# Kernel optimization log

Measured on AMD Instinct MI355X. Metric: run time of the kernel, lower is better.

## Reference

```python
import jax, jax.numpy as jnp
import numpy as np

N = 150000      # active voxels
C = 64          # head input channels
KK = 9          # 3x3 kernel offsets
H = W = 700     # BEV feature map
BN_EPS = 1e-5
HEADS = [("heatmap", 3), ("center", 2), ("center_z", 1), ("dim", 3), ("rot", 2)]


def _build_neighbor_table(seed=0):
    """Submanifold 3x3 neighbor indices for N active voxels on an HxW grid.
    Entry -1 means the neighbor site is inactive (contributes zero)."""
    rng = np.random.default_rng(seed)
    flat = rng.choice(H * W, size=N, replace=False)
    ys, xs = flat // W, flat % W
    lut = np.full(H * W, -1, np.int64)
    lut[flat] = np.arange(N)
    nbr = np.full((N, KK), -1, np.int64)
    k = 0
    for dy in (-1, 0, 1):
        for dx in (-1, 0, 1):
            ny, nx = ys + dy, xs + dx
            valid = (ny >= 0) & (ny < H) & (nx >= 0) & (nx < W)
            nf = np.where(valid, ny * W + nx, 0)
            nbr[:, k] = np.where(valid, lut[nf], -1)
            k += 1
    return nbr


def setup_inputs() -> dict:
    key = jax.random.key(0)
    ks = jax.random.split(key, 2 + 2 * len(HEADS))
    inp = {
        "features": jax.random.normal(ks[0], (N, C), jnp.float32),
        "nbr_idx": jnp.asarray(_build_neighbor_table(), jnp.int32),
        # one 3x3 subm conv per head, stacked: [n_heads, 9, C_in, C_out]
        "W3": jax.random.normal(ks[1], (len(HEADS), KK, C, C), jnp.float32) * 0.05,
        "gamma": jnp.ones((len(HEADS), C), jnp.float32),
        "beta": jnp.zeros((len(HEADS), C), jnp.float32),
    }
    for i, (name, oc) in enumerate(HEADS):
        inp[f"W1_{name}"] = jax.random.normal(ks[2 + i], (C, oc), jnp.float32) * 0.001
        if name == "heatmap":
            inp[f"b1_{name}"] = jnp.full((oc,), -float(np.log((1 - 0.01) / 0.01)), jnp.float32)
        else:
            inp[f"b1_{name}"] = jnp.zeros((oc,), jnp.float32)
    return inp


def _forward(features, nbr_idx, W3, gamma, beta, W1s, b1s):
    valid = nbr_idx >= 0                                  # [N, 9]
    idx = jnp.where(valid, nbr_idx, 0)
    # gather active-neighbor features; missing neighbors -> zero (subm conv)
    gathered = features[idx] * valid[..., None].astype(features.dtype)  # [N, 9, C]
    # all heads share the same input sparse tensor -> batched gather-GEMM
    h = jnp.einsum('nkc,hkco->hno', gathered, W3)         # [n_heads, N, C]
    # BatchNorm1d (training-mode batch stats, biased var) + ReLU
    mean = h.mean(axis=1, keepdims=True)
    var = ((h - mean) ** 2).mean(axis=1, keepdims=True)
    hn = (h - mean) * jax.lax.rsqrt(var + BN_EPS)
    hn = jax.nn.relu(hn * gamma[:, None, :] + beta[:, None, :])
    # per-head 1x1 subm conv == linear on active features
    return tuple(hn[i] @ W1s[i] + b1s[i] for i in range(len(HEADS)))


def reference(features, nbr_idx, W3, gamma, beta,
              W1_heatmap, b1_heatmap, W1_center, b1_center,
              W1_center_z, b1_center_z, W1_dim, b1_dim, W1_rot, b1_rot):
    W1s = [W1_heatmap, W1_center, W1_center_z, W1_dim, W1_rot]
    b1s = [b1_heatmap, b1_center, b1_center_z, b1_dim, b1_rot]
    return _forward(features, nbr_idx, W3, gamma, beta, W1s, b1s)
```

## Files before the change

kernel.cpp:

```cpp
#include <hip/hip_runtime.h>

#define NVOX 150000
#define BM 128
#define MTILES 1172
#define SROW 150016
#define NCOL 320

typedef __attribute__((ext_vector_type(8))) short bf16x8;
typedef __attribute__((ext_vector_type(4))) float f32x4;

__device__ __forceinline__ unsigned short f2bf(float f) {
    unsigned u = __builtin_bit_cast(unsigned, f);
    u += 0x7fffu + ((u >> 16) & 1u);
    return (unsigned short)(u >> 16);
}

__device__ __forceinline__ void gld16(const void* g, void* l) {
    __builtin_amdgcn_global_load_lds(
        (const __attribute__((address_space(1))) unsigned int*)g,
        (__attribute__((address_space(3))) unsigned int*)l, 16, 0, 0);
}

__global__ void prep_feat(const float* __restrict__ src, unsigned short* __restrict__ dst) {
    int i = blockIdx.x * 256 + threadIdx.x;
    if (i < NVOX * 8) {
        const float* s = src + (size_t)i * 8;
        float4 a = *(const float4*)s;
        float4 b = *(const float4*)(s + 4);
        union { bf16x8 v; unsigned short u[8]; } r;
        r.u[0] = f2bf(a.x); r.u[1] = f2bf(a.y); r.u[2] = f2bf(a.z); r.u[3] = f2bf(a.w);
        r.u[4] = f2bf(b.x); r.u[5] = f2bf(b.y); r.u[6] = f2bf(b.z); r.u[7] = f2bf(b.w);
        *(bf16x8*)(dst + (size_t)i * 8) = r.v;
    } else if (i < NVOX * 8 + 8) {
        bf16x8 z = {0, 0, 0, 0, 0, 0, 0, 0};
        *(bf16x8*)(dst + (size_t)i * 8) = z;
    }
}

__global__ void prep_w3(const float* __restrict__ w3, unsigned short* __restrict__ bt,
                        float* __restrict__ stats) {
    int i = blockIdx.x * 256 + threadIdx.x;
    int h = i / 36864;
    int rem = i - h * 36864;
    int kk = rem >> 12;
    int c = (rem >> 6) & 63;
    int o = rem & 63;
    bt[(size_t)(((h * 9 + kk) * 8) + (c >> 3)) * 512 + o * 8 + (c & 7)] = f2bf(w3[i]);
    if (i < 2 * NCOL) stats[i] = 0.f;
}

__global__ __launch_bounds__(512, 2)
void gemm_kernel(const unsigned short* __restrict__ featB,
                 const unsigned short* __restrict__ Bt2,
                 const int* __restrict__ nbr,
                 unsigned short* __restrict__ hbuf,
                 float* __restrict__ stats,
                 float* __restrict__ partials) {
    __shared__ __align__(16) char smem[119296];
    constexpr int SB_OFF = 32768;
    constexpr int IDX_OFF = 114688;
    constexpr int SRED_OFF = 88064;

    int mtile = blockIdx.x;
    int m0 = mtile * BM;

    int tid = threadIdx.x;
    int w = tid >> 6, lane = tid & 63;
    int quad = lane >> 4, m16 = lane & 15;

    for (int lin = tid; lin < BM * 9; lin += 512) {
        int row = lin / 9, kkq = lin - row * 9;
        int v = -1;
        if (m0 + row < NVOX) v = nbr[(size_t)(m0 + row) * 9 + kkq];
        *(int*)(smem + IDX_OFF + (kkq * BM + row) * 4) = ((v < 0) ? NVOX : v) * 128;
    }
    __syncthreads();

    f32x4 acc[4][5];
#pragma unroll
    for (int mt = 0; mt < 4; ++mt)
#pragma unroll
        for (int nt = 0; nt < 5; ++nt)
            acc[mt][nt] = (f32x4){0.f, 0.f, 0.f, 0.f};

    const char* fb = (const char*)featB;
    const char* bt = (const char*)Bt2;
    char* sAb[2] = {smem, smem + 16384};
    char* sBb[2] = {smem + SB_OFF, smem + SB_OFF + 40960};

    int mrow = (w >> 2) * 64;
    int cbase = (w & 3) * 80;

    int rloc = lane >> 3, j = lane & 7;
    int jx = (j ^ rloc) * 16;

    int bsj[5], bdj[5];
#pragma unroll
    for (int jj = 0; jj < 5; ++jj) {
        int u = w * 5 + jj;
        int h = u >> 3, c16 = u & 7;
        bsj[jj] = (h * 72 + c16) * 1024 + lane * 16;
        bdj[jj] = (h * 8 + c16) * 1024;
    }
    int sBoff[5];
#pragma unroll
    for (int nt = 0; nt < 5; ++nt) {
        int c = cbase + nt * 16 + m16;
        sBoff[nt] = (c >> 6) * 8192 + (c & 63) * 16;
    }
    int aRow[4];
#pragma unroll
    for (int mt = 0; mt < 4; ++mt)
        aRow[mt] = (mrow + mt * 16 + m16) * 128;
    int axor = m16 & 7;

    auto stage = [&](int buf, int kk) {
        char* sA = sAb[buf];
        char* sB = sBb[buf];
        int off0 = *(const int*)(smem + IDX_OFF + (kk * BM + w * 16 + rloc) * 4);
        int off1 = *(const int*)(smem + IDX_OFF + (kk * BM + w * 16 + 8 + rloc) * 4);
        gld16(fb + off0 + jx, sA + w * 2048);
        gld16(fb + off1 + jx, sA + w * 2048 + 1024);
#pragma unroll
        for (int jj = 0; jj < 5; ++jj)
            gld16(bt + (size_t)(bsj[jj] + kk * 8192), sB + bdj[jj]);
    };

    stage(0, 0);

#pragma unroll
    for (int kk = 0; kk < 9; ++kk) {
        const int p = kk & 1;
        if (kk < 8) {
            stage(p ^ 1, kk + 1);
            asm volatile("s_waitcnt vmcnt(7)" ::: "memory");
        } else {
            asm volatile("s_waitcnt vmcnt(0)" ::: "memory");
        }
        asm volatile("s_barrier" ::: "memory");
        __builtin_amdgcn_sched_barrier(0);
        __builtin_amdgcn_s_setprio(1);
#pragma unroll
        for (int ks = 0; ks < 2; ++ks) {
            bf16x8 af[4], bf[5];
            int xq = ((ks * 4 + quad) ^ axor) * 16;
#pragma unroll
            for (int mt = 0; mt < 4; ++mt)
                af[mt] = *(const bf16x8*)(sAb[p] + aRow[mt] + xq);
#pragma unroll
            for (int nt = 0; nt < 5; ++nt)
                bf[nt] = *(const bf16x8*)(sBb[p] + sBoff[nt] + (ks * 4 + quad) * 1024);
#pragma unroll
            for (int mt = 0; mt < 4; ++mt)
#pragma unroll
                for (int nt = 0; nt < 5; ++nt)
                    acc[mt][nt] = __builtin_amdgcn_mfma_f32_16x16x32_bf16(
                        af[mt], bf[nt], acc[mt][nt], 0, 0, 0);
        }
        __builtin_amdgcn_s_setprio(0);
        __builtin_amdgcn_sched_barrier(0);
        asm volatile("s_barrier" ::: "memory");
    }

#pragma unroll
    for (int mt = 0; mt < 4; ++mt) {
#pragma unroll
        for (int nt = 0; nt < 5; ++nt) {
            int col = cbase + nt * 16 + m16;
            int row = mrow + mt * 16 + quad * 4;
            f32x4 v = acc[mt][nt];
            unsigned lo = (unsigned)f2bf(v.x) | ((unsigned)f2bf(v.y) << 16);
            unsigned hi = (unsigned)f2bf(v.z) | ((unsigned)f2bf(v.w) << 16);
            uint2 pk; pk.x = lo; pk.y = hi;
            *(uint2*)(smem + col * 272 + row * 2) = pk;
        }
    }
    __syncthreads();
#pragma unroll
    for (int it = 0; it < 20; ++it) {
        int col = it * 16 + (tid >> 5);
        int l32 = tid & 31;
        uint2 v = *(const uint2*)(smem + col * 272 + l32 * 8);
        *(uint2*)(hbuf + (size_t)col * SROW + m0 + l32 * 4) = v;
    }

    float s[5], ss[5];
#pragma unroll
    for (int nt = 0; nt < 5; ++nt) {
        float a = 0.f, b = 0.f;
#pragma unroll
        for (int mt = 0; mt < 4; ++mt) {
            f32x4 v = acc[mt][nt];
            a += v.x + v.y + v.z + v.w;
            b += v.x * v.x + v.y * v.y + v.z * v.z + v.w * v.w;
        }
        s[nt] = a; ss[nt] = b;
        s[nt] += __shfl_xor(s[nt], 16); s[nt] += __shfl_xor(s[nt], 32);
        ss[nt] += __shfl_xor(ss[nt], 16); ss[nt] += __shfl_xor(ss[nt], 32);
    }
    if (quad == 0) {
#pragma unroll
        for (int nt = 0; nt < 5; ++nt) {
            float* p = (float*)(smem + SRED_OFF + (w * 80 + nt * 16 + m16) * 8);
            p[0] = s[nt]; p[1] = ss[nt];
        }
    }
    __syncthreads();
    if (tid < NCOL) {
        int c = tid;
        int qq = c / 80, lc = c - qq * 80;
        const float* p0 = (const float*)(smem + SRED_OFF + (qq * 80 + lc) * 8);
        const float* p1 = (const float*)(smem + SRED_OFF + ((qq + 4) * 80 + lc) * 8);
        float vsum = p0[0] + p1[0];
        float vss  = p0[1] + p1[1];
        if (partials) {
            float* pp = partials + (size_t)mtile * (2 * NCOL);
            pp[c] = vsum;
            pp[NCOL + c] = vss;
        } else {
            atomicAdd(&stats[c], vsum);
            atomicAdd(&stats[NCOL + c], vss);
        }
    }
}

__global__ __launch_bounds__(256)
void stats_reduce(const float* __restrict__ partials, float* __restrict__ stats) {
    __shared__ float red[256];
    int b = blockIdx.x;
    int tid = threadIdx.x;
    int cl = tid & 31;
    int chunk = tid >> 5;
    int jcol = b * 32 + cl;
    float s = 0.f;
    int m1 = chunk * 147 + 147; if (m1 > MTILES) m1 = MTILES;
    for (int m = chunk * 147; m < m1; ++m)
        s += partials[(size_t)m * (2 * NCOL) + jcol];
    red[tid] = s;
    __syncthreads();
    if (tid < 32) {
        float a = red[tid];
#pragma unroll
        for (int k = 1; k < 8; ++k) a += red[k * 32 + tid];
        stats[b * 32 + tid] = a;
    }
}

__global__ __launch_bounds__(256)
void head_kernel(const unsigned short* __restrict__ hbuf,
                 const float* __restrict__ stats,
                 const float* __restrict__ gamma, const float* __restrict__ beta,
                 const float* __restrict__ W1_0, const float* __restrict__ W1_1,
                 const float* __restrict__ W1_2, const float* __restrict__ W1_3,
                 const float* __restrict__ W1_4,
                 const float* __restrict__ b1_0, const float* __restrict__ b1_1,
                 const float* __restrict__ b1_2, const float* __restrict__ b1_3,
                 const float* __restrict__ b1_4,
                 float* __restrict__ out) {
    __shared__ float sScale[64], sShift[64], sW1[192], sB1[3];
    int h = blockIdx.y;
    const float* W1; const float* b1; int oc; size_t obase;
    if (h == 0)      { W1 = W1_0; b1 = b1_0; oc = 3; obase = 0; }
    else if (h == 1) { W1 = W1_1; b1 = b1_1; oc = 2; obase = 450000; }
    else if (h == 2) { W1 = W1_2; b1 = b1_2; oc = 1; obase = 750000; }
    else if (h == 3) { W1 = W1_3; b1 = b1_3; oc = 3; obase = 900000; }
    else             { W1 = W1_4; b1 = b1_4; oc = 2; obase = 1350000; }

    int tid = threadIdx.x;
    if (tid < 64) {
        int c = h * 64 + tid;
        float mean = stats[c] * (1.f / (float)NVOX);
        float var = stats[NCOL + c] * (1.f / (float)NVOX) - mean * mean;
        float inv = rsqrtf(var + 1e-5f);
        float sc = inv * gamma[c];
        sScale[tid] = sc;
        sShift[tid] = beta[c] - mean * sc;
    }
    for (int i = tid; i < 192; i += 256) {
        int cc = i / 3, jj = i - cc * 3;
        sW1[i] = (jj < oc) ? W1[cc * oc + jj] : 0.f;
    }
    if (tid == 0) {
        sB1[0] = b1[0];
        sB1[1] = (oc >= 2) ? b1[1] : 0.f;
        sB1[2] = (oc >= 3) ? b1[2] : 0.f;
    }
    __syncthreads();

    int n = (blockIdx.x * 256 + tid) * 4;
    if (n >= NVOX) return;
    const unsigned short* hp = hbuf + (size_t)(h * 64) * SROW + n;
    float x[4][3];
#pragma unroll
    for (int rr = 0; rr < 4; ++rr) { x[rr][0] = sB1[0]; x[rr][1] = sB1[1]; x[rr][2] = sB1[2]; }
#pragma unroll 8
    for (int cc = 0; cc < 64; ++cc) {
        uint2 raw = *(const uint2*)(hp + (size_t)cc * SROW);
        float sc = sScale[cc], sh = sShift[cc];
        float w0 = sW1[cc * 3 + 0], w1 = sW1[cc * 3 + 1], w2 = sW1[cc * 3 + 2];
        float v0 = __builtin_bit_cast(float, raw.x << 16);
        float v1 = __builtin_bit_cast(float, raw.x & 0xffff0000u);
        float v2 = __builtin_bit_cast(float, raw.y << 16);
        float v3 = __builtin_bit_cast(float, raw.y & 0xffff0000u);
        v0 = fmaxf(v0 * sc + sh, 0.f); v1 = fmaxf(v1 * sc + sh, 0.f);
        v2 = fmaxf(v2 * sc + sh, 0.f); v3 = fmaxf(v3 * sc + sh, 0.f);
        x[0][0] += v0 * w0; x[0][1] += v0 * w1; x[0][2] += v0 * w2;
        x[1][0] += v1 * w0; x[1][1] += v1 * w1; x[1][2] += v1 * w2;
        x[2][0] += v2 * w0; x[2][1] += v2 * w1; x[2][2] += v2 * w2;
        x[3][0] += v3 * w0; x[3][1] += v3 * w1; x[3][2] += v3 * w2;
    }
#pragma unroll
    for (int rr = 0; rr < 4; ++rr) {
        float* op = out + obase + (size_t)(n + rr) * oc;
        op[0] = x[rr][0];
        if (oc >= 2) op[1] = x[rr][1];
        if (oc >= 3) op[2] = x[rr][2];
    }
}

extern "C" void kernel_launch(void* const* d_in, const int* in_sizes, int n_in,
                              void* d_out, int out_size, void* d_ws, size_t ws_size,
                              hipStream_t stream) {
    const float* features = (const float*)d_in[0];
    const int* nbr        = (const int*)d_in[1];
    const float* w3       = (const float*)d_in[2];
    const float* gamma    = (const float*)d_in[3];
    const float* beta     = (const float*)d_in[4];
    const float* W1_0 = (const float*)d_in[5];  const float* b1_0 = (const float*)d_in[6];
    const float* W1_1 = (const float*)d_in[7];  const float* b1_1 = (const float*)d_in[8];
    const float* W1_2 = (const float*)d_in[9];  const float* b1_2 = (const float*)d_in[10];
    const float* W1_3 = (const float*)d_in[11]; const float* b1_3 = (const float*)d_in[12];
    const float* W1_4 = (const float*)d_in[13]; const float* b1_4 = (const float*)d_in[14];
    float* out = (float*)d_out;

    char* ws = (char*)d_ws;
    unsigned short* featB = (unsigned short*)ws;
    unsigned short* Bt2   = (unsigned short*)(ws + 19200128);
    float* stats          = (float*)(ws + 19568768);
    unsigned short* hbuf  = (unsigned short*)(ws + 19571328);
    constexpr size_t PART_OFF = 19571328 + (size_t)NCOL * SROW * 2;
    float* partials = nullptr;
    if (ws_size >= PART_OFF + (size_t)MTILES * 2 * NCOL * 4)
        partials = (float*)(ws + PART_OFF);

    prep_feat<<<(NVOX * 8 + 8 + 255) / 256, 256, 0, stream>>>(features, featB);
    prep_w3<<<184320 / 256, 256, 0, stream>>>(w3, Bt2, stats);
    gemm_kernel<<<MTILES, 512, 0, stream>>>(featB, Bt2, nbr, hbuf, stats, partials);
    if (partials)
        stats_reduce<<<20, 256, 0, stream>>>(partials, stats);
    head_kernel<<<dim3(147, 5), 256, 0, stream>>>(hbuf, stats, gamma, beta,
        W1_0, W1_1, W1_2, W1_3, W1_4, b1_0, b1_1, b1_2, b1_3, b1_4, out);
}
```

Measured before the change: 250.8 us.

## Store GEMM output row-major and read contiguous rows in head kernel

```diff
diff --git a/kernel.cpp b/kernel.cpp
--- a/kernel.cpp
+++ b/kernel.cpp
@@ -3,8 +3,8 @@
 #define NVOX 150000
 #define BM 128
 #define MTILES 1172
-#define SROW 150016
 #define NCOL 320
+#define HROWS 150016
 
 typedef __attribute__((ext_vector_type(8))) short bf16x8;
 typedef __attribute__((ext_vector_type(4))) float f32x4;
@@ -13,6 +13,10 @@
     unsigned u = __builtin_bit_cast(unsigned, f);
     u += 0x7fffu + ((u >> 16) & 1u);
     return (unsigned short)(u >> 16);
+}
+
+__device__ __forceinline__ float bf2f(unsigned short u) {
+    return __builtin_bit_cast(float, (unsigned)u << 16);
 }
 
 __device__ __forceinline__ void gld16(const void* g, void* l) {
@@ -59,7 +63,7 @@
     __shared__ __align__(16) char smem[119296];
     constexpr int SB_OFF = 32768;
     constexpr int IDX_OFF = 114688;
-    constexpr int SRED_OFF = 88064;
+    constexpr int SRED_OFF = 83968;
 
     int mtile = blockIdx.x;
     int m0 = mtile * BM;
@@ -155,7 +159,7 @@
 #pragma unroll
                 for (int nt = 0; nt < 5; ++nt)
                     acc[mt][nt] = __builtin_amdgcn_mfma_f32_16x16x32_bf16(
-                        af[mt], bf[nt], acc[mt][nt], 0, 0, 0);
+                        bf[nt], af[mt], acc[mt][nt], 0, 0, 0);
         }
         __builtin_amdgcn_s_setprio(0);
         __builtin_amdgcn_sched_barrier(0);
@@ -164,45 +168,52 @@
 
 #pragma unroll
     for (int mt = 0; mt < 4; ++mt) {
+        int row = mrow + mt * 16 + m16;
 #pragma unroll
         for (int nt = 0; nt < 5; ++nt) {
-            int col = cbase + nt * 16 + m16;
-            int row = mrow + mt * 16 + quad * 4;
+            int col0 = cbase + nt * 16 + quad * 4;
             f32x4 v = acc[mt][nt];
             unsigned lo = (unsigned)f2bf(v.x) | ((unsigned)f2bf(v.y) << 16);
             unsigned hi = (unsigned)f2bf(v.z) | ((unsigned)f2bf(v.w) << 16);
             uint2 pk; pk.x = lo; pk.y = hi;
-            *(uint2*)(smem + col * 272 + row * 2) = pk;
+            *(uint2*)(smem + row * 656 + col0 * 2) = pk;
         }
     }
     __syncthreads();
 #pragma unroll
     for (int it = 0; it < 20; ++it) {
-        int col = it * 16 + (tid >> 5);
-        int l32 = tid & 31;
-        uint2 v = *(const uint2*)(smem + col * 272 + l32 * 8);
-        *(uint2*)(hbuf + (size_t)col * SROW + m0 + l32 * 4) = v;
-    }
-
-    float s[5], ss[5];
+        int lin = it * 512 + tid;
+        int row = lin / 80, k = lin - row * 80;
+        uint2 v = *(const uint2*)(smem + row * 656 + k * 8);
+        *(uint2*)(hbuf + (size_t)(m0 + row) * NCOL + k * 4) = v;
+    }
+
 #pragma unroll
     for (int nt = 0; nt < 5; ++nt) {
-        float a = 0.f, b = 0.f;
+        float sj[4] = {0.f, 0.f, 0.f, 0.f}, ssj[4] = {0.f, 0.f, 0.f, 0.f};
 #pragma unroll
         for (int mt = 0; mt < 4; ++mt) {
             f32x4 v = acc[mt][nt];
-            a += v.x + v.y + v.z + v.w;
-            b += v.x * v.x + v.y * v.y + v.z * v.z + v.w * v.w;
-        }
-        s[nt] = a; ss[nt] = b;
-        s[nt] += __shfl_xor(s[nt], 16); s[nt] += __shfl_xor(s[nt], 32);
-        ss[nt] += __shfl_xor(ss[nt], 16); ss[nt] += __shfl_xor(ss[nt], 32);
-    }
-    if (quad == 0) {
-#pragma unroll
-        for (int nt = 0; nt < 5; ++nt) {
-            float* p = (float*)(smem + SRED_OFF + (w * 80 + nt * 16 + m16) * 8);
-            p[0] = s[nt]; p[1] = ss[nt];
+            sj[0] += v.x; ssj[0] += v.x * v.x;
+            sj[1] += v.y; ssj[1] += v.y * v.y;
+            sj[2] += v.z; ssj[2] += v.z * v.z;
+            sj[3] += v.w; ssj[3] += v.w * v.w;
+        }
+#pragma unroll
+        for (int jj = 0; jj < 4; ++jj) {
+#pragma unroll
+            for (int d = 1; d < 16; d <<= 1) {
+                sj[jj] += __shfl_xor(sj[jj], d);
+                ssj[jj] += __shfl_xor(ssj[jj], d);
+            }
+        }
+        if (m16 == 0) {
+#pragma unroll
+            for (int jj = 0; jj < 4; ++jj) {
+                float* p = (float*)(smem + SRED_OFF +
+                                    (w * 80 + nt * 16 + quad * 4 + jj) * 8);
+                p[0] = sj[jj]; p[1] = ssj[jj];
+            }
         }
     }
     __syncthreads();
@@ -227,14 +238,15 @@
 __global__ __launch_bounds__(256)
 void stats_reduce(const float* __restrict__ partials, float* __restrict__ stats) {
     __shared__ float red[256];
-    int b = blockIdx.x;
     int tid = threadIdx.x;
-    int cl = tid & 31;
-    int chunk = tid >> 5;
-    int jcol = b * 32 + cl;
+    int cl = tid & 31, sc = tid >> 5;
+    int jcol = blockIdx.x * 32 + cl;
+    int ybase = blockIdx.y * 147;
+    int mlo = ybase + sc * 19;
+    int mhi = ybase + 147; if (mhi > MTILES) mhi = MTILES;
+    int mend = mlo + 19; if (mend > mhi) mend = mhi;
     float s = 0.f;
-    int m1 = chunk * 147 + 147; if (m1 > MTILES) m1 = MTILES;
-    for (int m = chunk * 147; m < m1; ++m)
+    for (int m = mlo; m < mend; ++m)
         s += partials[(size_t)m * (2 * NCOL) + jcol];
     red[tid] = s;
     __syncthreads();
@@ -242,7 +254,7 @@
         float a = red[tid];
 #pragma unroll
         for (int k = 1; k < 8; ++k) a += red[k * 32 + tid];
-        stats[b * 32 + tid] = a;
+        atomicAdd(&stats[blockIdx.x * 32 + tid], a);
     }
 }
 
@@ -287,35 +299,30 @@
     }
     __syncthreads();
 
-    int n = (blockIdx.x * 256 + tid) * 4;
+    int n = blockIdx.x * 256 + tid;
     if (n >= NVOX) return;
-    const unsigned short* hp = hbuf + (size_t)(h * 64) * SROW + n;
-    float x[4][3];
-#pragma unroll
-    for (int rr = 0; rr < 4; ++rr) { x[rr][0] = sB1[0]; x[rr][1] = sB1[1]; x[rr][2] = sB1[2]; }
-#pragma unroll 8
-    for (int cc = 0; cc < 64; ++cc) {
-        uint2 raw = *(const uint2*)(hp + (size_t)cc * SROW);
-        float sc = sScale[cc], sh = sShift[cc];
-        float w0 = sW1[cc * 3 + 0], w1 = sW1[cc * 3 + 1], w2 = sW1[cc * 3 + 2];
-        float v0 = __builtin_bit_cast(float, raw.x << 16);
-        float v1 = __builtin_bit_cast(float, raw.x & 0xffff0000u);
-        float v2 = __builtin_bit_cast(float, raw.y << 16);
-        float v3 = __builtin_bit_cast(float, raw.y & 0xffff0000u);
-        v0 = fmaxf(v0 * sc + sh, 0.f); v1 = fmaxf(v1 * sc + sh, 0.f);
-        v2 = fmaxf(v2 * sc + sh, 0.f); v3 = fmaxf(v3 * sc + sh, 0.f);
-        x[0][0] += v0 * w0; x[0][1] += v0 * w1; x[0][2] += v0 * w2;
-        x[1][0] += v1 * w0; x[1][1] += v1 * w1; x[1][2] += v1 * w2;
-        x[2][0] += v2 * w0; x[2][1] += v2 * w1; x[2][2] += v2 * w2;
-        x[3][0] += v3 * w0; x[3][1] += v3 * w1; x[3][2] += v3 * w2;
-    }
-#pragma unroll
-    for (int rr = 0; rr < 4; ++rr) {
-        float* op = out + obase + (size_t)(n + rr) * oc;
-        op[0] = x[rr][0];
-        if (oc >= 2) op[1] = x[rr][1];
-        if (oc >= 3) op[2] = x[rr][2];
-    }
+    const unsigned short* hp = hbuf + (size_t)n * NCOL + h * 64;
+    bf16x8 r[8];
+#pragma unroll
+    for (int jv = 0; jv < 8; ++jv)
+        r[jv] = *(const bf16x8*)(hp + jv * 8);
+    float x0 = sB1[0], x1 = sB1[1], x2 = sB1[2];
+#pragma unroll
+    for (int jv = 0; jv < 8; ++jv) {
+#pragma unroll
+        for (int e = 0; e < 8; ++e) {
+            int cc = jv * 8 + e;
+            float v = bf2f((unsigned short)r[jv][e]);
+            v = fmaxf(v * sScale[cc] + sShift[cc], 0.f);
+            x0 += v * sW1[cc * 3 + 0];
+            x1 += v * sW1[cc * 3 + 1];
+            x2 += v * sW1[cc * 3 + 2];
+        }
+    }
+    float* op = out + obase + (size_t)n * oc;
+    op[0] = x0;
+    if (oc >= 2) op[1] = x1;
+    if (oc >= 3) op[2] = x2;
 }
 
 extern "C" void kernel_launch(void* const* d_in, const int* in_sizes, int n_in,
@@ -338,7 +345,7 @@
     unsigned short* Bt2   = (unsigned short*)(ws + 19200128);
     float* stats          = (float*)(ws + 19568768);
     unsigned short* hbuf  = (unsigned short*)(ws + 19571328);
-    constexpr size_t PART_OFF = 19571328 + (size_t)NCOL * SROW * 2;
+    constexpr size_t PART_OFF = 19571328 + (size_t)NCOL * HROWS * 2;
     float* partials = nullptr;
     if (ws_size >= PART_OFF + (size_t)MTILES * 2 * NCOL * 4)
         partials = (float*)(ws + PART_OFF);
@@ -347,7 +354,7 @@
     prep_w3<<<184320 / 256, 256, 0, stream>>>(w3, Bt2, stats);
     gemm_kernel<<<MTILES, 512, 0, stream>>>(featB, Bt2, nbr, hbuf, stats, partials);
     if (partials)
-        stats_reduce<<<20, 256, 0, stream>>>(partials, stats);
-    head_kernel<<<dim3(147, 5), 256, 0, stream>>>(hbuf, stats, gamma, beta,
+        stats_reduce<<<dim3(20, 8), 256, 0, stream>>>(partials, stats);
+    head_kernel<<<dim3((NVOX + 255) / 256, 5), 256, 0, stream>>>(hbuf, stats, gamma, beta,
         W1_0, W1_1, W1_2, W1_3, W1_4, b1_0, b1_1, b1_2, b1_3, b1_4, out);
 }
```

Result: faster. 236.8 us (-5.6%).

## Load GEMM weights into registers, merge prep kernels, parallelize stats reduction

Applied to the files above, without the earlier changes.

```diff
diff --git a/kernel.cpp b/kernel.cpp
--- a/kernel.cpp
+++ b/kernel.cpp
@@ -21,32 +21,34 @@
         (__attribute__((address_space(3))) unsigned int*)l, 16, 0, 0);
 }
 
-__global__ void prep_feat(const float* __restrict__ src, unsigned short* __restrict__ dst) {
-    int i = blockIdx.x * 256 + threadIdx.x;
-    if (i < NVOX * 8) {
-        const float* s = src + (size_t)i * 8;
-        float4 a = *(const float4*)s;
-        float4 b = *(const float4*)(s + 4);
-        union { bf16x8 v; unsigned short u[8]; } r;
-        r.u[0] = f2bf(a.x); r.u[1] = f2bf(a.y); r.u[2] = f2bf(a.z); r.u[3] = f2bf(a.w);
-        r.u[4] = f2bf(b.x); r.u[5] = f2bf(b.y); r.u[6] = f2bf(b.z); r.u[7] = f2bf(b.w);
-        *(bf16x8*)(dst + (size_t)i * 8) = r.v;
-    } else if (i < NVOX * 8 + 8) {
-        bf16x8 z = {0, 0, 0, 0, 0, 0, 0, 0};
-        *(bf16x8*)(dst + (size_t)i * 8) = z;
-    }
-}
-
-__global__ void prep_w3(const float* __restrict__ w3, unsigned short* __restrict__ bt,
-                        float* __restrict__ stats) {
-    int i = blockIdx.x * 256 + threadIdx.x;
-    int h = i / 36864;
-    int rem = i - h * 36864;
-    int kk = rem >> 12;
-    int c = (rem >> 6) & 63;
-    int o = rem & 63;
-    bt[(size_t)(((h * 9 + kk) * 8) + (c >> 3)) * 512 + o * 8 + (c & 7)] = f2bf(w3[i]);
-    if (i < 2 * NCOL) stats[i] = 0.f;
+__global__ void prep_all(const float* __restrict__ src, unsigned short* __restrict__ dst,
+                         const float* __restrict__ w3, unsigned short* __restrict__ bt,
+                         float* __restrict__ stats) {
+    int bid = blockIdx.x, tid = threadIdx.x;
+    if (bid < 4688) {
+        int i = bid * 256 + tid;
+        if (i < NVOX * 8) {
+            const float* s = src + (size_t)i * 8;
+            float4 a = *(const float4*)s;
+            float4 b = *(const float4*)(s + 4);
+            union { bf16x8 v; unsigned short u[8]; } r;
+            r.u[0] = f2bf(a.x); r.u[1] = f2bf(a.y); r.u[2] = f2bf(a.z); r.u[3] = f2bf(a.w);
+            r.u[4] = f2bf(b.x); r.u[5] = f2bf(b.y); r.u[6] = f2bf(b.z); r.u[7] = f2bf(b.w);
+            *(bf16x8*)(dst + (size_t)i * 8) = r.v;
+        } else if (i < NVOX * 8 + 8) {
+            bf16x8 z = {0, 0, 0, 0, 0, 0, 0, 0};
+            *(bf16x8*)(dst + (size_t)i * 8) = z;
+        }
+    } else {
+        int i = (bid - 4688) * 256 + tid;
+        int h = i / 36864;
+        int rem = i - h * 36864;
+        int kk = rem >> 12;
+        int c = (rem >> 6) & 63;
+        int o = rem & 63;
+        bt[(size_t)(((h * 9 + kk) * 8) + (c >> 3)) * 512 + o * 8 + (c & 7)] = f2bf(w3[i]);
+        if (i < 2 * NCOL) stats[i] = 0.f;
+    }
 }
 
 __global__ __launch_bounds__(512, 2)
@@ -56,9 +58,8 @@
                  unsigned short* __restrict__ hbuf,
                  float* __restrict__ stats,
                  float* __restrict__ partials) {
-    __shared__ __align__(16) char smem[119296];
-    constexpr int SB_OFF = 32768;
-    constexpr int IDX_OFF = 114688;
+    __shared__ __align__(16) char smem[93184];
+    constexpr int IDX_OFF = 32768;
     constexpr int SRED_OFF = 88064;
 
     int mtile = blockIdx.x;
@@ -86,7 +87,6 @@
     const char* fb = (const char*)featB;
     const char* bt = (const char*)Bt2;
     char* sAb[2] = {smem, smem + 16384};
-    char* sBb[2] = {smem + SB_OFF, smem + SB_OFF + 40960};
 
     int mrow = (w >> 2) * 64;
     int cbase = (w & 3) * 80;
@@ -94,19 +94,11 @@
     int rloc = lane >> 3, j = lane & 7;
     int jx = (j ^ rloc) * 16;
 
-    int bsj[5], bdj[5];
-#pragma unroll
-    for (int jj = 0; jj < 5; ++jj) {
-        int u = w * 5 + jj;
-        int h = u >> 3, c16 = u & 7;
-        bsj[jj] = (h * 72 + c16) * 1024 + lane * 16;
-        bdj[jj] = (h * 8 + c16) * 1024;
-    }
-    int sBoff[5];
+    int bOff[5];
 #pragma unroll
     for (int nt = 0; nt < 5; ++nt) {
         int c = cbase + nt * 16 + m16;
-        sBoff[nt] = (c >> 6) * 8192 + (c & 63) * 16;
+        bOff[nt] = (c >> 6) * 73728 + quad * 1024 + (c & 63) * 16;
     }
     int aRow[4];
 #pragma unroll
@@ -114,26 +106,33 @@
         aRow[mt] = (mrow + mt * 16 + m16) * 128;
     int axor = m16 & 7;
 
-    auto stage = [&](int buf, int kk) {
+    bf16x8 breg[2][2][5];
+
+    auto stageA = [&](int buf, int kk) {
         char* sA = sAb[buf];
-        char* sB = sBb[buf];
         int off0 = *(const int*)(smem + IDX_OFF + (kk * BM + w * 16 + rloc) * 4);
         int off1 = *(const int*)(smem + IDX_OFF + (kk * BM + w * 16 + 8 + rloc) * 4);
         gld16(fb + off0 + jx, sA + w * 2048);
         gld16(fb + off1 + jx, sA + w * 2048 + 1024);
-#pragma unroll
-        for (int jj = 0; jj < 5; ++jj)
-            gld16(bt + (size_t)(bsj[jj] + kk * 8192), sB + bdj[jj]);
     };
-
-    stage(0, 0);
+    auto loadB = [&](int p, int kk) {
+#pragma unroll
+        for (int nt = 0; nt < 5; ++nt) {
+            breg[p][0][nt] = *(const bf16x8*)(bt + (size_t)(bOff[nt] + kk * 8192));
+            breg[p][1][nt] = *(const bf16x8*)(bt + (size_t)(bOff[nt] + kk * 8192 + 4096));
+        }
+    };
+
+    stageA(0, 0);
+    loadB(0, 0);
 
 #pragma unroll
     for (int kk = 0; kk < 9; ++kk) {
         const int p = kk & 1;
         if (kk < 8) {
-            stage(p ^ 1, kk + 1);
-            asm volatile("s_waitcnt vmcnt(7)" ::: "memory");
+            stageA(p ^ 1, kk + 1);
+            loadB(p ^ 1, kk + 1);
+            asm volatile("s_waitcnt vmcnt(12)" ::: "memory");
         } else {
             asm volatile("s_waitcnt vmcnt(0)" ::: "memory");
         }
@@ -142,25 +141,23 @@
         __builtin_amdgcn_s_setprio(1);
 #pragma unroll
         for (int ks = 0; ks < 2; ++ks) {
-            bf16x8 af[4], bf[5];
+            bf16x8 af[4];
             int xq = ((ks * 4 + quad) ^ axor) * 16;
 #pragma unroll
             for (int mt = 0; mt < 4; ++mt)
                 af[mt] = *(const bf16x8*)(sAb[p] + aRow[mt] + xq);
 #pragma unroll
-            for (int nt = 0; nt < 5; ++nt)
-                bf[nt] = *(const bf16x8*)(sBb[p] + sBoff[nt] + (ks * 4 + quad) * 1024);
-#pragma unroll
             for (int mt = 0; mt < 4; ++mt)
 #pragma unroll
                 for (int nt = 0; nt < 5; ++nt)
                     acc[mt][nt] = __builtin_amdgcn_mfma_f32_16x16x32_bf16(
-                        af[mt], bf[nt], acc[mt][nt], 0, 0, 0);
+                        af[mt], breg[p][ks][nt], acc[mt][nt], 0, 0, 0);
         }
         __builtin_amdgcn_s_setprio(0);
         __builtin_amdgcn_sched_barrier(0);
         asm volatile("s_barrier" ::: "memory");
     }
+    __builtin_amdgcn_sched_barrier(0);
 
 #pragma unroll
     for (int mt = 0; mt < 4; ++mt) {
@@ -227,14 +224,15 @@
 __global__ __launch_bounds__(256)
 void stats_reduce(const float* __restrict__ partials, float* __restrict__ stats) {
     __shared__ float red[256];
-    int b = blockIdx.x;
     int tid = threadIdx.x;
-    int cl = tid & 31;
-    int chunk = tid >> 5;
-    int jcol = b * 32 + cl;
+    int cl = tid & 31, sc = tid >> 5;
+    int jcol = blockIdx.x * 32 + cl;
+    int ybase = blockIdx.y * 147;
+    int mlo = ybase + sc * 19;
+    int mhi = ybase + 147; if (mhi > MTILES) mhi = MTILES;
+    int mend = mlo + 19; if (mend > mhi) mend = mhi;
     float s = 0.f;
-    int m1 = chunk * 147 + 147; if (m1 > MTILES) m1 = MTILES;
-    for (int m = chunk * 147; m < m1; ++m)
+    for (int m = mlo; m < mend; ++m)
         s += partials[(size_t)m * (2 * NCOL) + jcol];
     red[tid] = s;
     __syncthreads();
@@ -242,7 +240,7 @@
         float a = red[tid];
 #pragma unroll
         for (int k = 1; k < 8; ++k) a += red[k * 32 + tid];
-        stats[b * 32 + tid] = a;
+        atomicAdd(&stats[blockIdx.x * 32 + tid], a);
     }
 }
 
@@ -343,11 +341,10 @@
     if (ws_size >= PART_OFF + (size_t)MTILES * 2 * NCOL * 4)
         partials = (float*)(ws + PART_OFF);
 
-    prep_feat<<<(NVOX * 8 + 8 + 255) / 256, 256, 0, stream>>>(features, featB);
-    prep_w3<<<184320 / 256, 256, 0, stream>>>(w3, Bt2, stats);
+    prep_all<<<4688 + 720, 256, 0, stream>>>(features, featB, w3, Bt2, stats);
     gemm_kernel<<<MTILES, 512, 0, stream>>>(featB, Bt2, nbr, hbuf, stats, partials);
     if (partials)
-        stats_reduce<<<20, 256, 0, stream>>>(partials, stats);
+        stats_reduce<<<dim3(20, 8), 256, 0, stream>>>(partials, stats);
     head_kernel<<<dim3(147, 5), 256, 0, stream>>>(hbuf, stats, gamma, beta,
         W1_0, W1_1, W1_2, W1_3, W1_4, b1_0, b1_1, b1_2, b1_3, b1_4, out);
 }
```

Result: faster. 224.3 us (-10.5%).
